# Kernel optimization log

Hardware: AMD Instinct MI355X
Metric: run time of the kernel (lower is better)

Reference implementation:

```python
import jax, jax.numpy as jnp
import numpy as np

NP = 16  # num_patches per side (init kwarg)


def setup_inputs() -> dict:
    key = jax.random.key(0)
    ks = jax.random.split(key, 8)
    B, C, H, W = 16, 16, 256, 256
    ph, pw = H // NP, W // NP          # 16, 16
    D = C * ph * pw                     # in_channels = 4096
    E = 512                             # embedding_dim
    s = 0.02
    return {
        "x": jax.random.normal(ks[0], (B, C, H, W), dtype=jnp.float32),
        "theta_w": jax.random.normal(ks[1], (D, E), dtype=jnp.float32) * s,
        "theta_b": jnp.zeros((E,), dtype=jnp.float32),
        "f_w": jax.random.normal(ks[2], (D, E), dtype=jnp.float32) * s,
        "f_b": jnp.zeros((E,), dtype=jnp.float32),
        "g_w": jax.random.normal(ks[3], (D, D), dtype=jnp.float32) * s,
        "g_b": jnp.zeros((D,), dtype=jnp.float32),
        "scale": jnp.ones((1,), dtype=jnp.float32),
    }


def reference(x, theta_w, theta_b, f_w, f_b, g_w, g_b, scale):
    B, C, H, W = x.shape
    ph, pw = H // NP, W // NP
    P = NP * NP                 # number of patches (== ph*pw by construction)
    D = C * ph * pw             # flattened patch dim = in_channels
    # extract non-overlapping patches: [B,C,H,W] -> [B,P,D] (C,ph,pw order)
    p = (x.reshape(B, C, NP, ph, NP, pw)
           .transpose(0, 2, 4, 1, 3, 5)
           .reshape(B, P, D))
    theta = p @ theta_w + theta_b                         # [B,P,E]
    f = p @ f_w + f_b                                     # [B,P,E]
    weights = jax.nn.softmax(
        jnp.einsum('bpe,bqe->bpq', theta, f), axis=-1)    # [B,P,P]
    g = (p @ g_w + g_b).reshape(B, P, C, ph * pw)         # [B,P,C,N], N==P
    # broadcast gate (NOT a matmul combine): weights.unsqueeze(2) * g
    enhanced = weights[:, :, None, :] * g                 # [B,P,C,N]
    img = (enhanced.reshape(B, NP, NP, C, ph, pw)
                   .transpose(0, 3, 1, 4, 2, 5)
                   .reshape(B, C, H, W))
    return scale * img + x
```

## Files before the change

kernel.cpp:

```cpp
#include <hip/hip_runtime.h>
#include <hip/hip_bf16.h>
#include <stdint.h>


typedef __hip_bfloat16 bf16;
typedef __bf16 bf16x8 __attribute__((ext_vector_type(8)));
typedef float f32x4 __attribute__((ext_vector_type(4)));

#define GLOBAL_AS __attribute__((address_space(1)))
#define LDS_AS __attribute__((address_space(3)))

__device__ __forceinline__ void gload_lds16(const void* g, void* l) {
    void* gg = const_cast<void*>(g);
    __builtin_amdgcn_global_load_lds((GLOBAL_AS void*)gg, (LDS_AS void*)l, 16, 0, 0);
}


__global__ __launch_bounds__(256) void prep_pw(const float* __restrict__ x,
                                               const float* __restrict__ theta_w,
                                               const float* __restrict__ f_w,
                                               bf16* __restrict__ pHi,
                                               bf16* __restrict__ pLo,
                                               bf16* __restrict__ wHi,
                                               bf16* __restrict__ wLo) {
    __shared__ float tile[32][33];
    int blk = blockIdx.x;
    if (blk < 16384) {
        int tid = blk * 256 + threadIdx.x;
        int w4 = tid & 63;
        int h  = (tid >> 6) & 255;
        int c  = (tid >> 14) & 15;
        int b  = tid >> 18;
        float4 v = ((const float4*)x)[tid];
        int i = h >> 4, y = h & 15, j = w4 >> 2, zb = (w4 & 3) * 4;
        int m = b * 256 + i * 16 + j;
        int k = c * 256 + y * 16 + zb;
        size_t o = (size_t)m * 4096 + k;
        float vs[4] = {v.x, v.y, v.z, v.w};
#pragma unroll
        for (int q = 0; q < 4; ++q) {
            bf16 hv = __float2bfloat16(vs[q]);
            float rem = vs[q] - __bfloat162float(hv);
            pHi[o + q] = hv;
            pLo[o + q] = __float2bfloat16(rem);
        }
    } else {
        int bid = blk - 16384;
        int t = threadIdx.x;
        int tx = t & 31, ty = t >> 5;
        int k0 = (bid & 127) * 32;
        int e0 = (bid >> 7) * 32;
#pragma unroll
        for (int r = 0; r < 4; ++r) {
            int k = k0 + ty + r * 8;
            int e = e0 + tx;
            float v = (e < 512) ? theta_w[(size_t)k * 512 + e]
                                : f_w[(size_t)k * 512 + (e - 512)];
            tile[ty + r * 8][tx] = v;
        }
        __syncthreads();
#pragma unroll
        for (int r = 0; r < 4; ++r) {
            int e = e0 + ty + r * 8;
            int k = k0 + tx;
            float v = tile[tx][ty + r * 8];
            bf16 hv = __float2bfloat16(v);
            float rem = v - __bfloat162float(hv);
            wHi[(size_t)e * 4096 + k] = hv;
            wLo[(size_t)e * 4096 + k] = __float2bfloat16(rem);
        }
    }
}

__device__ __forceinline__ void gemm_pass(const bf16* A, const bf16* Bt,
                                          int lda, int ldb, int m0, int n0,
                                          int kbase, int ksteps,
                                          bf16* As, bf16* Bs, f32x4 (&acc)[4][4]) {
    int t = threadIdx.x, lane = t & 63, wave = t >> 6;
    int wm = wave & 1, wn = wave >> 1;
    int lr = lane & 15, lq = lane >> 4;
    const bf16* gA = A + (size_t)m0 * lda;
    const bf16* gB = Bt + (size_t)n0 * ldb;
    int chunk0 = wave * 2;
    int srow0 = lane >> 2;
    int cb = (lane & 3) * 16;
    for (int ks = 0; ks < ksteps; ++ks) {
        int kt = kbase + ks * 32;
#pragma unroll
        for (int tt = 0; tt < 2; ++tt) {
            int chunk = chunk0 + tt;
            int row = chunk * 16 + srow0;
            gload_lds16((const char*)(gA + ((size_t)row * lda + kt)) + cb,
                        (char*)As + chunk * 1024);
            gload_lds16((const char*)(gB + ((size_t)row * ldb + kt)) + cb,
                        (char*)Bs + chunk * 1024);
        }
        __syncthreads();
        bf16x8 af[4], bfr[4];
#pragma unroll
        for (int mt = 0; mt < 4; ++mt)
            af[mt] = *(const bf16x8*)((const char*)As + (wm * 64 + mt * 16 + lr) * 64 + lq * 16);
#pragma unroll
        for (int nt = 0; nt < 4; ++nt)
            bfr[nt] = *(const bf16x8*)((const char*)Bs + (wn * 64 + nt * 16 + lr) * 64 + lq * 16);
#pragma unroll
        for (int mt = 0; mt < 4; ++mt)
#pragma unroll
            for (int nt = 0; nt < 4; ++nt)
                acc[mt][nt] = __builtin_amdgcn_mfma_f32_16x16x32_bf16(
                    af[mt], bfr[nt], acc[mt][nt], 0, 0, 0);
        __syncthreads();
    }
}


__global__ __launch_bounds__(256) void gemm1f(const bf16* __restrict__ pHi,
                                              const bf16* __restrict__ pLo,
                                              const bf16* __restrict__ wHi,
                                              const bf16* __restrict__ wLo,
                                              float* __restrict__ C1a,
                                              float* __restrict__ C1b) {
    __shared__ bf16 AsHi[128 * 32];
    __shared__ bf16 AsLo[128 * 32];
    __shared__ bf16 BsHi[128 * 32];
    __shared__ bf16 BsLo[128 * 32];
    int m0 = blockIdx.x * 128;
    int n0 = blockIdx.y * 128;
    int kbase = blockIdx.z * 2048;
    int t = threadIdx.x, lane = t & 63, wave = t >> 6;
    int wm = wave & 1, wn = wave >> 1;
    int lr = lane & 15, lq = lane >> 4;
    const bf16* gAh = wHi + (size_t)m0 * 4096;
    const bf16* gAl = wLo + (size_t)m0 * 4096;
    const bf16* gBh = pHi + (size_t)n0 * 4096;
    const bf16* gBl = pLo + (size_t)n0 * 4096;
    int chunk0 = wave * 2;
    int srow0 = lane >> 2;
    int cb = (lane & 3) * 16;
    f32x4 acc[4][4] = {};
    for (int ks = 0; ks < 64; ++ks) {
        int kt = kbase + ks * 32;
#pragma unroll
        for (int tt = 0; tt < 2; ++tt) {
            int chunk = chunk0 + tt;
            size_t off = (size_t)(chunk * 16 + srow0) * 4096 + kt;
            gload_lds16((const char*)(gAh + off) + cb, (char*)AsHi + chunk * 1024);
            gload_lds16((const char*)(gAl + off) + cb, (char*)AsLo + chunk * 1024);
            gload_lds16((const char*)(gBh + off) + cb, (char*)BsHi + chunk * 1024);
            gload_lds16((const char*)(gBl + off) + cb, (char*)BsLo + chunk * 1024);
        }
        __syncthreads();
        bf16x8 ah[4], al[4], bh[4], bl[4];
#pragma unroll
        for (int mt = 0; mt < 4; ++mt) {
            int ro = (wm * 64 + mt * 16 + lr) * 64 + lq * 16;
            ah[mt] = *(const bf16x8*)((const char*)AsHi + ro);
            al[mt] = *(const bf16x8*)((const char*)AsLo + ro);
        }
#pragma unroll
        for (int nt = 0; nt < 4; ++nt) {
            int ro = (wn * 64 + nt * 16 + lr) * 64 + lq * 16;
            bh[nt] = *(const bf16x8*)((const char*)BsHi + ro);
            bl[nt] = *(const bf16x8*)((const char*)BsLo + ro);
        }
#pragma unroll
        for (int mt = 0; mt < 4; ++mt)
#pragma unroll
            for (int nt = 0; nt < 4; ++nt)
                acc[mt][nt] = __builtin_amdgcn_mfma_f32_16x16x32_bf16(
                    ah[mt], bl[nt], acc[mt][nt], 0, 0, 0);
#pragma unroll
        for (int mt = 0; mt < 4; ++mt)
#pragma unroll
            for (int nt = 0; nt < 4; ++nt)
                acc[mt][nt] = __builtin_amdgcn_mfma_f32_16x16x32_bf16(
                    al[mt], bh[nt], acc[mt][nt], 0, 0, 0);
#pragma unroll
        for (int mt = 0; mt < 4; ++mt)
#pragma unroll
            for (int nt = 0; nt < 4; ++nt)
                acc[mt][nt] = __builtin_amdgcn_mfma_f32_16x16x32_bf16(
                    ah[mt], bh[nt], acc[mt][nt], 0, 0, 0);
        __syncthreads();
    }
    float* C = blockIdx.z ? C1b : C1a;
#pragma unroll
    for (int mt = 0; mt < 4; ++mt) {
        int e = m0 + wm * 64 + mt * 16 + lq * 4;
#pragma unroll
        for (int nt = 0; nt < 4; ++nt) {
            int p = n0 + wn * 64 + nt * 16 + lr;
            *(float4*)(C + (size_t)p * 1024 + e) = *(float4*)&acc[mt][nt];
        }
    }
}


__global__ __launch_bounds__(256) void combine_prepg(const float* __restrict__ C1a,
                                                     const float* __restrict__ C1b,
                                                     const float* __restrict__ theta_b,
                                                     const float* __restrict__ f_b,
                                                     const float* __restrict__ g_w,
                                                     bf16* __restrict__ thfHi,
                                                     bf16* __restrict__ thfLo,
                                                     bf16* __restrict__ gwt) {
    __shared__ float tile[32][33];
    int blk = blockIdx.x;
    if (blk < 4096) {
        int id = blk * 256 + threadIdx.x;
        int c4 = id & 255;
        float4 va = ((const float4*)C1a)[id];
        float4 vb = ((const float4*)C1b)[id];
        float vs[4] = {va.x + vb.x, va.y + vb.y, va.z + vb.z, va.w + vb.w};
        union { ushort4 u; unsigned short s[4]; } H, L;
#pragma unroll
        for (int q = 0; q < 4; ++q) {
            int col = c4 * 4 + q;
            float bias = (col < 512) ? theta_b[col] : f_b[col - 512];
            float v = vs[q] + bias;
            bf16 h = __float2bfloat16(v);
            float rem = v - __bfloat162float(h);
            bf16 l = __float2bfloat16(rem);
            H.s[q] = *(unsigned short*)&h;
            L.s[q] = *(unsigned short*)&l;
        }
        ((ushort4*)thfHi)[id] = H.u;
        ((ushort4*)thfLo)[id] = L.u;
    } else {
        int bid = blk - 4096;
        int t = threadIdx.x;
        int tx = t & 31, ty = t >> 5;
        int k0 = (bid & 127) * 32;
        int n0 = (bid >> 7) * 32;
#pragma unroll
        for (int r = 0; r < 4; ++r) {
            int k = k0 + ty + r * 8;
            tile[ty + r * 8][tx] = g_w[(size_t)k * 4096 + (n0 + tx)];
        }
        __syncthreads();
#pragma unroll
        for (int r = 0; r < 4; ++r) {
            int n = n0 + ty + r * 8;
            int k = k0 + tx;
            gwt[(size_t)n * 4096 + k] = __float2bfloat16(tile[tx][ty + r * 8]);
        }
    }
}


__global__ __launch_bounds__(256, 3) void scores(const bf16* __restrict__ thfHi,
                                                 const bf16* __restrict__ thfLo,
                                                 float* __restrict__ S) {
    __shared__ bf16 As[128 * 32];
    __shared__ bf16 Bs[128 * 32];
    int m0 = blockIdx.x * 128;
    int n0 = blockIdx.y * 128;
    int b = blockIdx.z;
    const bf16* Ahi = thfHi + (size_t)b * 256 * 1024;
    const bf16* Alo = thfLo + (size_t)b * 256 * 1024;
    f32x4 acc[4][4] = {};
    gemm_pass(Ahi + 512, Ahi, 1024, 1024, m0, n0, 0, 16, As, Bs, acc);
    gemm_pass(Ahi + 512, Alo, 1024, 1024, m0, n0, 0, 16, As, Bs, acc);
    gemm_pass(Alo + 512, Ahi, 1024, 1024, m0, n0, 0, 16, As, Bs, acc);
    float* Sb = S + (size_t)b * 65536;
    int t = threadIdx.x, lane = t & 63, wave = t >> 6;
    int wm = wave & 1, wn = wave >> 1;
    int lr = lane & 15, lq = lane >> 4;
#pragma unroll
    for (int mt = 0; mt < 4; ++mt) {
        int q = m0 + wm * 64 + mt * 16 + lq * 4;
#pragma unroll
        for (int nt = 0; nt < 4; ++nt) {
            int p = n0 + wn * 64 + nt * 16 + lr;
            *(float4*)(Sb + (size_t)p * 256 + q) = *(float4*)&acc[mt][nt];
        }
    }
}


__global__ __launch_bounds__(256) void softmax_rows(float* __restrict__ S) {
    int row = blockIdx.x * 4 + (threadIdx.x >> 6);
    int lane = threadIdx.x & 63;
    float4* p = (float4*)(S + (size_t)row * 256);
    float4 v = p[lane];
    float mx = fmaxf(fmaxf(v.x, v.y), fmaxf(v.z, v.w));
#pragma unroll
    for (int s = 32; s >= 1; s >>= 1) mx = fmaxf(mx, __shfl_xor(mx, s, 64));
    v.x = expf(v.x - mx); v.y = expf(v.y - mx);
    v.z = expf(v.z - mx); v.w = expf(v.w - mx);
    float sm = (v.x + v.y) + (v.z + v.w);
#pragma unroll
    for (int s = 32; s >= 1; s >>= 1) sm += __shfl_xor(sm, s, 64);
    float inv = 1.0f / sm;
    v.x *= inv; v.y *= inv; v.z *= inv; v.w *= inv;
    p[lane] = v;
}


__global__ __launch_bounds__(256, 4) void gemm2(const bf16* __restrict__ pHi,
                                                const bf16* __restrict__ gwt,
                                                const float* __restrict__ g_b,
                                                const float* __restrict__ wts,
                                                const float* __restrict__ x,
                                                const float* __restrict__ scale,
                                                float* __restrict__ out) {
    __shared__ bf16 As[128 * 32];
    __shared__ bf16 Bs[128 * 32];
    int m0 = blockIdx.x * 128;
    int n0 = blockIdx.y * 128;
    f32x4 acc[4][4] = {};
    gemm_pass(gwt, pHi, 4096, 4096, m0, n0, 0, 128, As, Bs, acc);
    int t = threadIdx.x, lane = t & 63, wave = t >> 6;
    int wm = wave & 1, wn = wave >> 1;
    int lr = lane & 15, lq = lane >> 4;
    float scl = scale[0];
#pragma unroll
    for (int mt = 0; mt < 4; ++mt) {
        int ng = m0 + wm * 64 + mt * 16 + lq * 4;
        int cc = ng >> 8;
        int y = (ng >> 4) & 15;
        int zq = ng & 255;
        float4 gb4 = *(const float4*)(g_b + ng);
#pragma unroll
        for (int nt = 0; nt < 4; ++nt) {
            int mg = n0 + wn * 64 + nt * 16 + lr;
            int bb = mg >> 8, pi = mg & 255;
            int i = pi >> 4, j = pi & 15;
            float4 wt4 = *(const float4*)(wts + (size_t)mg * 256 + zq);
            size_t idx = ((((size_t)(bb * 16 + cc)) * 256) + i * 16 + y) * 256
                         + j * 16 + (ng & 15);
            float4 xv = *(const float4*)(x + idx);
            f32x4 a = acc[mt][nt];
            float4 o;
            o.x = scl * wt4.x * (a[0] + gb4.x) + xv.x;
            o.y = scl * wt4.y * (a[1] + gb4.y) + xv.y;
            o.z = scl * wt4.z * (a[2] + gb4.z) + xv.z;
            o.w = scl * wt4.w * (a[3] + gb4.w) + xv.w;
            *(float4*)(out + idx) = o;
        }
    }
}


extern "C" void kernel_launch(void* const* d_in, const int* in_sizes, int n_in,
                              void* d_out, int out_size, void* d_ws, size_t ws_size,
                              hipStream_t stream) {
    const float* x       = (const float*)d_in[0];
    const float* theta_w = (const float*)d_in[1];
    const float* theta_b = (const float*)d_in[2];
    const float* f_w     = (const float*)d_in[3];
    const float* f_b     = (const float*)d_in[4];
    const float* g_w     = (const float*)d_in[5];
    const float* g_b     = (const float*)d_in[6];
    const float* scale   = (const float*)d_in[7];
    (void)in_sizes; (void)n_in; (void)out_size; (void)ws_size;

    const size_t MiB = 1048576;
    char* ws = (char*)d_ws;
    bf16*  pHi   = (bf16*)(ws);
    bf16*  pLo   = (bf16*)(ws + 32 * MiB);
    bf16*  gwt   = (bf16*)(ws + 32 * MiB);
    bf16*  wHi   = (bf16*)(ws + 64 * MiB);
    bf16*  wLo   = (bf16*)(ws + 72 * MiB);
    bf16*  thfHi = (bf16*)(ws + 64 * MiB);
    bf16*  thfLo = (bf16*)(ws + 72 * MiB);
    float* C1a   = (float*)(ws + 80 * MiB);
    float* S     = (float*)(ws + 80 * MiB);
    float* C1b   = (float*)(ws + 96 * MiB);

    prep_pw<<<20480, 256, 0, stream>>>(x, theta_w, f_w, pHi, pLo, wHi, wLo);
    gemm1f<<<dim3(8, 32, 2), 256, 0, stream>>>(pHi, pLo, wHi, wLo, C1a, C1b);
    combine_prepg<<<20480, 256, 0, stream>>>(C1a, C1b, theta_b, f_b, g_w,
                                             thfHi, thfLo, gwt);
    scores<<<dim3(2, 2, 16), 256, 0, stream>>>(thfHi, thfLo, S);
    softmax_rows<<<1024, 256, 0, stream>>>(S);
    gemm2<<<dim3(32, 32), 256, 0, stream>>>(pHi, gwt, g_b, S, x, scale, (float*)d_out);
}
```

Measured before the change: 527.0 us.

## Vectorize patch-split stores and shrink gemm1f M-tile to raise occupancy

```diff
diff --git a/kernel.cpp b/kernel.cpp
--- a/kernel.cpp
+++ b/kernel.cpp
@@ -6,6 +6,7 @@
 typedef __hip_bfloat16 bf16;
 typedef __bf16 bf16x8 __attribute__((ext_vector_type(8)));
 typedef float f32x4 __attribute__((ext_vector_type(4)));
+typedef unsigned short u16x8 __attribute__((ext_vector_type(8)));
 
 #define GLOBAL_AS __attribute__((address_space(1)))
 #define LDS_AS __attribute__((address_space(3)))
@@ -13,6 +14,11 @@
 __device__ __forceinline__ void gload_lds16(const void* g, void* l) {
     void* gg = const_cast<void*>(g);
     __builtin_amdgcn_global_load_lds((GLOBAL_AS void*)gg, (LDS_AS void*)l, 16, 0, 0);
+}
+
+__device__ __forceinline__ unsigned short bf16_bits(float v) {
+    bf16 h = __float2bfloat16(v);
+    return *(unsigned short*)&h;
 }
 
 
@@ -25,28 +31,36 @@
                                                bf16* __restrict__ wLo) {
     __shared__ float tile[32][33];
     int blk = blockIdx.x;
-    if (blk < 16384) {
-        int tid = blk * 256 + threadIdx.x;
-        int w4 = tid & 63;
-        int h  = (tid >> 6) & 255;
-        int c  = (tid >> 14) & 15;
-        int b  = tid >> 18;
-        float4 v = ((const float4*)x)[tid];
-        int i = h >> 4, y = h & 15, j = w4 >> 2, zb = (w4 & 3) * 4;
-        int m = b * 256 + i * 16 + j;
-        int k = c * 256 + y * 16 + zb;
-        size_t o = (size_t)m * 4096 + k;
-        float vs[4] = {v.x, v.y, v.z, v.w};
+    int t = threadIdx.x;
+    if (blk < 4096) {
+        int m = blk;
+        int b = m >> 8, pi = m & 255;
+        int i = pi >> 4, j = pi & 15;
+        int c = t >> 4, y = t & 15;
+        const float* xr = x + ((((size_t)(b * 16 + c)) * 256 + i * 16 + y) * 256
+                               + j * 16);
+        float vv[16];
 #pragma unroll
         for (int q = 0; q < 4; ++q) {
-            bf16 hv = __float2bfloat16(vs[q]);
-            float rem = vs[q] - __bfloat162float(hv);
-            pHi[o + q] = hv;
-            pLo[o + q] = __float2bfloat16(rem);
-        }
+            float4 v = ((const float4*)xr)[q];
+            vv[q * 4 + 0] = v.x; vv[q * 4 + 1] = v.y;
+            vv[q * 4 + 2] = v.z; vv[q * 4 + 3] = v.w;
+        }
+        unsigned short h[16], l[16];
+#pragma unroll
+        for (int q = 0; q < 16; ++q) {
+            bf16 hv = __float2bfloat16(vv[q]);
+            float rem = vv[q] - __bfloat162float(hv);
+            h[q] = *(unsigned short*)&hv;
+            l[q] = bf16_bits(rem);
+        }
+        size_t o = (size_t)m * 4096 + t * 16;
+        *(u16x8*)(pHi + o)     = *(u16x8*)h;
+        *(u16x8*)(pHi + o + 8) = *(u16x8*)(h + 8);
+        *(u16x8*)(pLo + o)     = *(u16x8*)l;
+        *(u16x8*)(pLo + o + 8) = *(u16x8*)(l + 8);
     } else {
-        int bid = blk - 16384;
-        int t = threadIdx.x;
+        int bid = blk - 4096;
         int tx = t & 31, ty = t >> 5;
         int k0 = (bid & 127) * 32;
         int e0 = (bid >> 7) * 32;
@@ -114,71 +128,77 @@
 }
 
 
-__global__ __launch_bounds__(256) void gemm1f(const bf16* __restrict__ pHi,
-                                              const bf16* __restrict__ pLo,
-                                              const bf16* __restrict__ wHi,
-                                              const bf16* __restrict__ wLo,
-                                              float* __restrict__ C1a,
-                                              float* __restrict__ C1b) {
-    __shared__ bf16 AsHi[128 * 32];
-    __shared__ bf16 AsLo[128 * 32];
+__global__ __launch_bounds__(256, 4) void gemm1f(const bf16* __restrict__ pHi,
+                                                 const bf16* __restrict__ pLo,
+                                                 const bf16* __restrict__ wHi,
+                                                 const bf16* __restrict__ wLo,
+                                                 float* __restrict__ C1a,
+                                                 float* __restrict__ C1b) {
+    __shared__ bf16 AsHi[64 * 32];
+    __shared__ bf16 AsLo[64 * 32];
     __shared__ bf16 BsHi[128 * 32];
     __shared__ bf16 BsLo[128 * 32];
-    int m0 = blockIdx.x * 128;
+    int m0 = blockIdx.x * 64;
     int n0 = blockIdx.y * 128;
     int kbase = blockIdx.z * 2048;
     int t = threadIdx.x, lane = t & 63, wave = t >> 6;
-    int wm = wave & 1, wn = wave >> 1;
     int lr = lane & 15, lq = lane >> 4;
     const bf16* gAh = wHi + (size_t)m0 * 4096;
     const bf16* gAl = wLo + (size_t)m0 * 4096;
     const bf16* gBh = pHi + (size_t)n0 * 4096;
     const bf16* gBl = pLo + (size_t)n0 * 4096;
-    int chunk0 = wave * 2;
     int srow0 = lane >> 2;
     int cb = (lane & 3) * 16;
-    f32x4 acc[4][4] = {};
+    f32x4 acc[4][2] = {};
     for (int ks = 0; ks < 64; ++ks) {
         int kt = kbase + ks * 32;
 #pragma unroll
-        for (int tt = 0; tt < 2; ++tt) {
-            int chunk = chunk0 + tt;
-            size_t off = (size_t)(chunk * 16 + srow0) * 4096 + kt;
-            gload_lds16((const char*)(gAh + off) + cb, (char*)AsHi + chunk * 1024);
-            gload_lds16((const char*)(gAl + off) + cb, (char*)AsLo + chunk * 1024);
-            gload_lds16((const char*)(gBh + off) + cb, (char*)BsHi + chunk * 1024);
-            gload_lds16((const char*)(gBl + off) + cb, (char*)BsLo + chunk * 1024);
-        }
-        __syncthreads();
-        bf16x8 ah[4], al[4], bh[4], bl[4];
+        for (int tt = 0; tt < 6; ++tt) {
+            int chunk = wave * 6 + tt;
+            const bf16* src;
+            char* dst;
+            if (chunk < 8) {
+                int c2 = chunk & 3;
+                src = (chunk < 4 ? gAh : gAl) + (size_t)(c2 * 16 + srow0) * 4096 + kt;
+                dst = (char*)(chunk < 4 ? AsHi : AsLo) + c2 * 1024;
+            } else {
+                int c2 = (chunk - 8) & 7;
+                bool hi = chunk < 16;
+                src = (hi ? gBh : gBl) + (size_t)(c2 * 16 + srow0) * 4096 + kt;
+                dst = (char*)(hi ? BsHi : BsLo) + c2 * 1024;
+            }
+            gload_lds16((const char*)src + cb, dst);
+        }
+        __syncthreads();
+        bf16x8 ah[4], al[4], bh[2], bl[2];
 #pragma unroll
         for (int mt = 0; mt < 4; ++mt) {
-            int ro = (wm * 64 + mt * 16 + lr) * 64 + lq * 16;
+            int ro = (mt * 16 + lr) * 64 + lq * 16;
             ah[mt] = *(const bf16x8*)((const char*)AsHi + ro);
             al[mt] = *(const bf16x8*)((const char*)AsLo + ro);
         }
 #pragma unroll
-        for (int nt = 0; nt < 4; ++nt) {
-            int ro = (wn * 64 + nt * 16 + lr) * 64 + lq * 16;
+        for (int nt = 0; nt < 2; ++nt) {
+            int ro = (wave * 32 + nt * 16 + lr) * 64 + lq * 16;
             bh[nt] = *(const bf16x8*)((const char*)BsHi + ro);
             bl[nt] = *(const bf16x8*)((const char*)BsLo + ro);
         }
 #pragma unroll
         for (int mt = 0; mt < 4; ++mt)
 #pragma unroll
-            for (int nt = 0; nt < 4; ++nt)
+            for (int nt = 0; nt < 2; ++nt)
                 acc[mt][nt] = __builtin_amdgcn_mfma_f32_16x16x32_bf16(
                     ah[mt], bl[nt], acc[mt][nt], 0, 0, 0);
 #pragma unroll
         for (int mt = 0; mt < 4; ++mt)
 #pragma unroll
-            for (int nt = 0; nt < 4; ++nt)
+            for (int nt = 0; nt < 2; ++nt)
                 acc[mt][nt] = __builtin_amdgcn_mfma_f32_16x16x32_bf16(
                     al[mt], bh[nt], acc[mt][nt], 0, 0, 0);
 #pragma unroll
         for (int mt = 0; mt < 4; ++mt)
 #pragma unroll
-            for (int nt = 0; nt < 4; ++nt)
+            for (int nt = 0; nt < 2; ++nt)
                 acc[mt][nt] = __builtin_amdgcn_mfma_f32_16x16x32_bf16(
                     ah[mt], bh[nt], acc[mt][nt], 0, 0, 0);
         __syncthreads();
@@ -186,10 +206,10 @@
     float* C = blockIdx.z ? C1b : C1a;
 #pragma unroll
     for (int mt = 0; mt < 4; ++mt) {
-        int e = m0 + wm * 64 + mt * 16 + lq * 4;
-#pragma unroll
-        for (int nt = 0; nt < 4; ++nt) {
-            int p = n0 + wn * 64 + nt * 16 + lr;
+        int e = m0 + mt * 16 + lq * 4;
+#pragma unroll
+        for (int nt = 0; nt < 2; ++nt) {
+            int p = n0 + wave * 32 + nt * 16 + lr;
             *(float4*)(C + (size_t)p * 1024 + e) = *(float4*)&acc[mt][nt];
         }
     }
@@ -368,8 +388,8 @@
     float* S     = (float*)(ws + 80 * MiB);
     float* C1b   = (float*)(ws + 96 * MiB);
 
-    prep_pw<<<20480, 256, 0, stream>>>(x, theta_w, f_w, pHi, pLo, wHi, wLo);
-    gemm1f<<<dim3(8, 32, 2), 256, 0, stream>>>(pHi, pLo, wHi, wLo, C1a, C1b);
+    prep_pw<<<8192, 256, 0, stream>>>(x, theta_w, f_w, pHi, pLo, wHi, wLo);
+    gemm1f<<<dim3(16, 32, 2), 256, 0, stream>>>(pHi, pLo, wHi, wLo, C1a, C1b);
     combine_prepg<<<20480, 256, 0, stream>>>(C1a, C1b, theta_b, f_b, g_w,
                                              thfHi, thfLo, gwt);
     scores<<<dim3(2, 2, 16), 256, 0, stream>>>(thfHi, thfLo, S);
```

After: 569.5 us. 1.08x slower.
